# Optimization experiments

Hardware: AMD Instinct MI355X
Metric: run time of the kernel (lower is better)

The kernel has to match this reference:

```python
import jax, jax.numpy as jnp
import numpy as np

NUM_BLOCKS = 16
IN_FEATURES = 4096
OUT_FEATURES = 4096
BLOCK_IN = IN_FEATURES // NUM_BLOCKS
BLOCK_OUT = OUT_FEATURES // NUM_BLOCKS
BATCH = 16384


def setup_inputs() -> dict:
    key = jax.random.key(0)
    kx, kw, kb = jax.random.split(key, 3)
    x = jax.random.normal(kx, (BATCH, IN_FEATURES), dtype=jnp.float32)
    # Per-block weights, matching torch nn.Linear init scale (U[-1/sqrt(in), 1/sqrt(in)])
    bound = 1.0 / np.sqrt(BLOCK_IN)
    W = jax.random.uniform(kw, (NUM_BLOCKS, BLOCK_OUT, BLOCK_IN), minval=-bound, maxval=bound, dtype=jnp.float32)
    b = jax.random.uniform(kb, (NUM_BLOCKS, BLOCK_OUT), minval=-bound, maxval=bound, dtype=jnp.float32)
    return {"x": x, "W": W, "b": b}


def reference(x, W, b):
    # x: [N, in_features] -> [N, nb, block_in]
    n = x.shape[0]
    xb = x.reshape(n, NUM_BLOCKS, BLOCK_IN)
    # per-block linear: y = x @ W_k.T + b_k  (fused block-diagonal GEMM)
    yb = jnp.einsum('nki,koi->nko', xb, W) + b  # [N, nb, block_out]
    return yb.reshape(n, OUT_FEATURES)
```

## Files before the change

kernel.cpp:

```cpp
#include <hip/hip_runtime.h>

typedef short short8 __attribute__((ext_vector_type(8)));
typedef float floatx4 __attribute__((ext_vector_type(4)));
typedef unsigned uint2v __attribute__((ext_vector_type(2)));

#define INF 4096
#define TROWS 32
#define RS 528
#define TB (TROWS * RS)

__device__ __forceinline__ ushort f2bf(float f) {
  unsigned u = __builtin_bit_cast(unsigned, f);
  u += 0x7fffu + ((u >> 16) & 1u);
  return (ushort)(u >> 16);
}

__global__ __launch_bounds__(512, 1) void bd_gemm(
    const float* __restrict__ x, const float* __restrict__ W,
    const float* __restrict__ bias, float* __restrict__ out)
{
  __shared__ __align__(16) char xlds[2 * TB];

  const int bid  = blockIdx.x;
  const int kb   = bid & 15;
  const int mg   = bid >> 4;
  const int tid  = threadIdx.x;
  const int lane = tid & 63;
  const int w    = tid >> 6;
  const int ln   = lane & 15;
  const int lk   = lane >> 4;

  const float* xbase = x   + (size_t)(mg * 1024) * INF + kb * 256;
  float*       obase = out + (size_t)(mg * 1024) * INF + kb * 256 + w * 32;

#define LGKM0_BAR()                                                           \
  do {                                                                        \
    asm volatile("s_waitcnt lgkmcnt(0)" ::: "memory");                        \
    __builtin_amdgcn_s_barrier();                                             \
    asm volatile("" ::: "memory");                                            \
  } while (0)

  floatx4 g[4];

#define LOADX(t)                                                              \
  _Pragma("unroll") for (int i_ = 0; i_ < 4; ++i_)                            \
    g[i_] = *(const floatx4*)(xbase + (size_t)((t) * TROWS + w * 4 + i_) * INF + lane * 4);

#define WRITEX(t)                                                             \
  _Pragma("unroll") for (int i_ = 0; i_ < 4; ++i_) {                          \
    const int r_ = w * 4 + i_;                                                \
    unsigned p0_, p1_;                                                        \
    asm("v_cvt_pk_bf16_f32 %0, %1, %2" : "=v"(p0_) : "v"(g[i_][0]), "v"(g[i_][1])); \
    asm("v_cvt_pk_bf16_f32 %0, %1, %2" : "=v"(p1_) : "v"(g[i_][2]), "v"(g[i_][3])); \
    uint2v u_; u_[0] = p0_; u_[1] = p1_;                                      \
    *(uint2v*)(xlds + ((t) & 1) * TB + r_ * RS + lane * 8) = u_;              \
  }

#define COMPUTE(t)                                                            \
  {                                                                           \
    const char* bb_ = xlds + ((t) & 1) * TB;                                  \
    _Pragma("unroll") for (int a_ = 0; a_ < 4; ++a_)                          \
      _Pragma("unroll") for (int e_ = 0; e_ < 4; ++e_) acc[a_][e_] = 0.0f;    \
    _Pragma("unroll") for (int kc_ = 0; kc_ < 8; ++kc_) {                     \
      short8 xf_[2];                                                          \
      _Pragma("unroll") for (int mi_ = 0; mi_ < 2; ++mi_)                     \
        xf_[mi_] = *(const short8*)(bb_ + (mi_ * 16 + ln) * RS + kc_ * 64 + lk * 16); \
      _Pragma("unroll") for (int mi_ = 0; mi_ < 2; ++mi_)                     \
        _Pragma("unroll") for (int ni_ = 0; ni_ < 2; ++ni_)                   \
          acc[mi_ * 2 + ni_] = __builtin_amdgcn_mfma_f32_16x16x32_bf16(       \
              wf[ni_][kc_], xf_[mi_], acc[mi_ * 2 + ni_], 0, 0, 0);           \
    }                                                                         \
  }

#define STOREACC(t)                                                           \
  _Pragma("unroll") for (int mi_ = 0; mi_ < 2; ++mi_)                         \
    _Pragma("unroll") for (int ni_ = 0; ni_ < 2; ++ni_) {                     \
      floatx4 r_ = acc[mi_ * 2 + ni_];                                        \
      _Pragma("unroll") for (int j_ = 0; j_ < 4; ++j_) r_[j_] += bv[ni_][j_]; \
      *(floatx4*)(obase + (size_t)((t) * TROWS + mi_ * 16 + ln) * INF +       \
                  ni_ * 16 + lk * 4) = r_;                                    \
    }

  LOADX(0)

  short8 wf[2][8];
  {
    const float* wp = W + (size_t)kb * 65536 + (w * 32 + ln) * 256 + lk * 8;
#pragma unroll
    for (int ni = 0; ni < 2; ++ni)
#pragma unroll
      for (int kc = 0; kc < 8; ++kc) {
        const float* s = wp + ni * 16 * 256 + kc * 32;
        floatx4 v0 = *(const floatx4*)s;
        floatx4 v1 = *(const floatx4*)(s + 4);
        short8 u;
#pragma unroll
        for (int j = 0; j < 4; ++j) {
          u[j]     = (short)f2bf(v0[j]);
          u[4 + j] = (short)f2bf(v1[j]);
        }
        wf[ni][kc] = u;
      }
  }
  floatx4 bv[2];
#pragma unroll
  for (int ni = 0; ni < 2; ++ni)
    bv[ni] = *(const floatx4*)(bias + kb * 256 + w * 32 + ni * 16 + lk * 4);

  floatx4 acc[4];

  WRITEX(0)
  LGKM0_BAR();

#pragma unroll 1
  for (int t = 0; t < 32; ++t) {
    if (t < 31) LOADX(t + 1)
    COMPUTE(t)
    STOREACC(t)
    if (t < 31) {
      WRITEX(t + 1)
      LGKM0_BAR();
    }
  }

#undef LGKM0_BAR
#undef LOADX
#undef WRITEX
#undef COMPUTE
#undef STOREACC
}

extern "C" void kernel_launch(void* const* d_in, const int* in_sizes, int n_in,
                              void* d_out, int out_size, void* d_ws, size_t ws_size,
                              hipStream_t stream) {
  const float* x = (const float*)d_in[0];
  const float* W = (const float*)d_in[1];
  const float* b = (const float*)d_in[2];
  float* out = (float*)d_out;
  hipLaunchKernelGGL(bd_gemm, dim3(256), dim3(512), 0, stream, x, W, b, out);
}
```

Before: 108.5 us.

## Stage x tiles via global_load_lds triple buffer with LDS-side bf16 conversion

Replaces the register-staged global loads of x with direct global-to-LDS loads into a three-deep fp32 ring buffer, prefetched three tiles ahead. A separate conversion pass then reads fp32 from LDS, packs it to bf16 into the double-buffered padded tile, and feeds the MFMAs. The goal is deeper memory latency hiding and lower register pressure from in-flight loads. In exchange it uses much more LDS, adds an extra LDS read/write pass, and relies on exact vmcnt counting, since global stores are counted too.

```diff
diff --git a/kernel.cpp b/kernel.cpp
--- a/kernel.cpp
+++ b/kernel.cpp
@@ -6,8 +6,10 @@
 
 #define INF 4096
 #define TROWS 32
+#define FTB (TROWS * 1024)
 #define RS 528
-#define TB (TROWS * RS)
+#define BTB (TROWS * RS)
+#define BF16OFF (3 * FTB)
 
 __device__ __forceinline__ ushort f2bf(float f) {
   unsigned u = __builtin_bit_cast(unsigned, f);
@@ -19,7 +21,7 @@
     const float* __restrict__ x, const float* __restrict__ W,
     const float* __restrict__ bias, float* __restrict__ out)
 {
-  __shared__ __align__(16) char xlds[2 * TB];
+  __shared__ __align__(16) char xlds[3 * FTB + 2 * BTB];
 
   const int bid  = blockIdx.x;
   const int kb   = bid & 15;
@@ -33,6 +35,7 @@
   const float* xbase = x   + (size_t)(mg * 1024) * INF + kb * 256;
   float*       obase = out + (size_t)(mg * 1024) * INF + kb * 256 + w * 32;
 
+#define WAITVM(N) asm volatile("s_waitcnt vmcnt(" #N ")" ::: "memory")
 #define LGKM0_BAR()                                                           \
   do {                                                                        \
     asm volatile("s_waitcnt lgkmcnt(0)" ::: "memory");                        \
@@ -40,25 +43,35 @@
     asm volatile("" ::: "memory");                                            \
   } while (0)
 
-  floatx4 g[4];
-
-#define LOADX(t)                                                              \
-  _Pragma("unroll") for (int i_ = 0; i_ < 4; ++i_)                            \
-    g[i_] = *(const floatx4*)(xbase + (size_t)((t) * TROWS + w * 4 + i_) * INF + lane * 4);
-
-#define WRITEX(t)                                                             \
+#define PREFETCH(t)                                                           \
   _Pragma("unroll") for (int i_ = 0; i_ < 4; ++i_) {                          \
     const int r_ = w * 4 + i_;                                                \
-    unsigned p0_, p1_;                                                        \
-    asm("v_cvt_pk_bf16_f32 %0, %1, %2" : "=v"(p0_) : "v"(g[i_][0]), "v"(g[i_][1])); \
-    asm("v_cvt_pk_bf16_f32 %0, %1, %2" : "=v"(p1_) : "v"(g[i_][2]), "v"(g[i_][3])); \
-    uint2v u_; u_[0] = p0_; u_[1] = p1_;                                      \
-    *(uint2v*)(xlds + ((t) & 1) * TB + r_ * RS + lane * 8) = u_;              \
+    const float* gp_ = xbase + (size_t)((t) * TROWS + r_) * INF + lane * 4;   \
+    __builtin_amdgcn_global_load_lds(                                         \
+        (const __attribute__((address_space(1))) float*)gp_,                  \
+        (__attribute__((address_space(3))) float*)(                           \
+            xlds + ((t) % 3) * FTB + r_ * 1024),                              \
+        16, 0, 0);                                                            \
+  }
+
+#define CVT(t)                                                                \
+  {                                                                           \
+    const char* fb_ = xlds + ((t) % 3) * FTB;                                 \
+    char*       ob_ = xlds + BF16OFF + ((t) & 1) * BTB;                       \
+    _Pragma("unroll") for (int i_ = 0; i_ < 4; ++i_) {                        \
+      const int r_ = w * 4 + i_;                                              \
+      floatx4 v_ = *(const floatx4*)(fb_ + r_ * 1024 + lane * 16);            \
+      unsigned p0_, p1_;                                                      \
+      asm("v_cvt_pk_bf16_f32 %0, %1, %2" : "=v"(p0_) : "v"(v_[0]), "v"(v_[1])); \
+      asm("v_cvt_pk_bf16_f32 %0, %1, %2" : "=v"(p1_) : "v"(v_[2]), "v"(v_[3])); \
+      uint2v u_; u_[0] = p0_; u_[1] = p1_;                                    \
+      *(uint2v*)(ob_ + r_ * RS + lane * 8) = u_;                              \
+    }                                                                         \
   }
 
 #define COMPUTE(t)                                                            \
   {                                                                           \
-    const char* bb_ = xlds + ((t) & 1) * TB;                                  \
+    const char* bb_ = xlds + BF16OFF + ((t) & 1) * BTB;                       \
     _Pragma("unroll") for (int a_ = 0; a_ < 4; ++a_)                          \
       _Pragma("unroll") for (int e_ = 0; e_ < 4; ++e_) acc[a_][e_] = 0.0f;    \
     _Pragma("unroll") for (int kc_ = 0; kc_ < 8; ++kc_) {                     \
@@ -81,7 +94,7 @@
                   ni_ * 16 + lk * 4) = r_;                                    \
     }
 
-  LOADX(0)
+  PREFETCH(0) PREFETCH(1) PREFETCH(2)
 
   short8 wf[2][8];
   {
@@ -109,23 +122,45 @@
 
   floatx4 acc[4];
 
-  WRITEX(0)
+  WAITVM(4);
+  CVT(0)
+
   LGKM0_BAR();
+  PREFETCH(3)
+  CVT(1)
+  COMPUTE(0)
+  STOREACC(0)
+  WAITVM(8); LGKM0_BAR();
+  PREFETCH(4)
+  CVT(2)
+  COMPUTE(1)
+  STOREACC(1)
 
 #pragma unroll 1
-  for (int t = 0; t < 32; ++t) {
-    if (t < 31) LOADX(t + 1)
+  for (int t = 2; t <= 28; ++t) {
+    WAITVM(12); LGKM0_BAR();
+    PREFETCH(t + 3)
+    CVT(t + 1)
     COMPUTE(t)
     STOREACC(t)
-    if (t < 31) {
-      WRITEX(t + 1)
-      LGKM0_BAR();
-    }
   }
 
+  WAITVM(12); LGKM0_BAR();
+  CVT(30)
+  COMPUTE(29)
+  STOREACC(29)
+  WAITVM(8); LGKM0_BAR();
+  CVT(31)
+  COMPUTE(30)
+  STOREACC(30)
+  LGKM0_BAR();
+  COMPUTE(31)
+  STOREACC(31)
+
+#undef WAITVM
 #undef LGKM0_BAR
-#undef LOADX
-#undef WRITEX
+#undef PREFETCH
+#undef CVT
 #undef COMPUTE
 #undef STOREACC
 }
```

Result: slower. 114.2 us (+5.2%).
